# Performance work log

Measured on AMD Instinct MI355X. Metric: run time of the kernel, lower is better.

The kernel has to match this reference:

```python
import jax, jax.numpy as jnp
import numpy as np
import math

B, L, HID, H = 16, 1024, 1024, 16
E = HID // H
HALF = L // 2 + 1                      # 513 rfft bins
GLOBAL_RATIO = 0.6
LEFT = int(HALF * (1.0 - GLOBAL_RATIO))  # 205 (i=0, filter_mixer='G')
RIGHT = HALF                            # 513
FACTOR = 1
TOP_K = int(FACTOR * math.log(L))       # 6
LN_EPS = 1e-12


def setup_inputs() -> dict:
    key = jax.random.key(0)
    ks = jax.random.split(key, 12)
    s = 0.02
    return {
        "input_tensor": jax.random.normal(ks[0], (B, L, HID), jnp.float32),
        "attention_mask": jnp.zeros((B, 1, 1, L), jnp.float32),
        "Wq": jax.random.normal(ks[1], (HID, HID), jnp.float32) * s,
        "bq": jnp.zeros((HID,), jnp.float32),
        "Wk": jax.random.normal(ks[2], (HID, HID), jnp.float32) * s,
        "bk": jnp.zeros((HID,), jnp.float32),
        "Wv": jax.random.normal(ks[3], (HID, HID), jnp.float32) * s,
        "bv": jnp.zeros((HID,), jnp.float32),
        "Wd": jax.random.normal(ks[4], (HID, HID), jnp.float32) * s,
        "bd": jnp.zeros((HID,), jnp.float32),
        "gamma": jnp.ones((HID,), jnp.float32),
        "beta": jnp.zeros((HID,), jnp.float32),
    }


def _heads(x):  # [B,L,HID] -> [B,H,E,L]
    return x.reshape(B, L, H, E).transpose(0, 2, 3, 1)


def _layer_norm(x, gamma, beta):
    mu = jnp.mean(x, axis=-1, keepdims=True)
    var = jnp.var(x, axis=-1, keepdims=True)
    return (x - mu) / jnp.sqrt(var + LN_EPS) * gamma + beta


def reference(input_tensor, attention_mask, Wq, bq, Wk, bk, Wv, bv, Wd, bd, gamma, beta):
    # QKV projections -> [B,H,E,L]
    q = _heads(input_tensor @ Wq + bq)
    k = _heads(input_tensor @ Wk + bk)
    v = _heads(input_tensor @ Wv + bv)

    # FFT-based autocorrelation restricted to retained frequency band [LEFT,RIGHT)
    q_fft = jnp.fft.rfft(q, axis=-1)            # [B,H,E,HALF] complex64
    k_fft = jnp.fft.rfft(k, axis=-1)
    res = q_fft[..., LEFT:RIGHT] * jnp.conj(k_fft[..., LEFT:RIGHT])
    box = jnp.zeros((B, H, E, HALF), res.dtype).at[..., LEFT:RIGHT].set(res)
    corr = jnp.fft.irfft(box, n=L, axis=-1)     # [B,H,E,L]

    # time_delay_agg_training: topk shared delays, softmax-weighted roll aggregation
    mean_value = jnp.mean(corr, axis=(1, 2))            # [B,L]
    _, idx = jax.lax.top_k(jnp.mean(mean_value, axis=0), TOP_K)  # [TOP_K]
    weights = mean_value[:, idx]                         # [B,TOP_K]
    tmp_corr = jax.nn.softmax(weights, axis=-1)
    delays_agg = jnp.zeros_like(v)
    for i in range(TOP_K):  # TOP_K=6, fixed small loop
        pattern = jnp.roll(v, -idx[i], axis=-1)
        delays_agg = delays_agg + pattern * tmp_corr[:, i][:, None, None, None]

    # [B,H,E,L] -> [B,L,HID]
    context = delays_agg.transpose(0, 3, 1, 2).reshape(B, L, HID)
    hidden = context @ Wd + bd
    return _layer_norm(hidden + input_tensor, gamma, beta)
```

## Files before the change

### kernel.cpp

```cpp
#include <hip/hip_runtime.h>


typedef unsigned short u16;
typedef unsigned int   u32;
typedef __attribute__((ext_vector_type(8))) __bf16 bf16x8;
typedef __attribute__((ext_vector_type(4))) float  floatx4;

#define HIDn 1024

__device__ __forceinline__ u16 f2b(float f){ u32 i = __float_as_uint(f); return (u16)((i + 0x7fffu + ((i>>16)&1u)) >> 16); }

__device__ __forceinline__ void gl_lds16(const u16* g, u16* l){
  __builtin_amdgcn_global_load_lds((__attribute__((address_space(1))) const void*)g,
                                   (__attribute__((address_space(3))) void*)l, 16, 0, 0);
}

__device__ __forceinline__ void bar(){
  asm volatile("" ::: "memory");
  __builtin_amdgcn_s_barrier();
  asm volatile("" ::: "memory");
}
__device__ __forceinline__ void lgkm0(){
  asm volatile("s_waitcnt lgkmcnt(0)" ::: "memory");
  __builtin_amdgcn_sched_barrier(0);
}

__global__ void fill_kernel(float* __restrict__ out, float v, int n)
{
  const int i = blockIdx.x*blockDim.x + threadIdx.x;
  if (i < n) out[i] = v;
}

__global__ __launch_bounds__(256)
void cast_kernel(const float* __restrict__ x, u16* __restrict__ xb)
{
  const int i = blockIdx.x*256 + threadIdx.x;
  const float4* xp = (const float4*)x;
  const float4 a = xp[2*i], b = xp[2*i+1];
  uint4 o;
  o.x = (u32)f2b(a.x) | ((u32)f2b(a.y)<<16);
  o.y = (u32)f2b(a.z) | ((u32)f2b(a.w)<<16);
  o.z = (u32)f2b(b.x) | ((u32)f2b(b.y)<<16);
  o.w = (u32)f2b(b.z) | ((u32)f2b(b.w)<<16);
  ((uint4*)xb)[i] = o;
}

__global__ __launch_bounds__(1024)
void transpose_kernel(const float* __restrict__ Wq, const float* __restrict__ Wk,
                      const float* __restrict__ Wv, const float* __restrict__ Wd,
                      u16* __restrict__ WqkvT, u16* __restrict__ WdT)
{
  __shared__ float tile[32][33];
  const int mat = blockIdx.z;
  const float* W = (mat==0)?Wq:(mat==1)?Wk:(mat==2)?Wv:Wd;
  const int k = blockIdx.y*32 + threadIdx.y;
  const int n = blockIdx.x*32 + threadIdx.x;
  tile[threadIdx.y][threadIdx.x] = W[(long)k*HIDn + n];
  __syncthreads();
  const int on = blockIdx.x*32 + threadIdx.y;
  const int ok = blockIdx.y*32 + threadIdx.x;
  const u16 val = f2b(tile[threadIdx.x][threadIdx.y]);
  if (mat < 3) WqkvT[(long)(mat*HIDn + on)*HIDn + ok] = val;
  else         WdT[(long)on*HIDn + ok] = val;
}

__global__ __launch_bounds__(1024)
void gf_kernel(float* __restrict__ gf, float* __restrict__ c)
{
  const int d = threadIdx.x;
  float s = 0.f;
  for (int f = 205; f < 512; ++f){
    int p = (f*d) & 1023;
    s += cosf(6.283185307179586f * (float)p * (1.0f/1024.0f));
  }
  gf[d] = (2.f*s + ((d & 1) ? -1.f : 1.f)) * (1.0f/1048576.0f);
  #pragma unroll
  for (int b = 0; b < 16; ++b) c[b*1024 + d] = 0.f;
}

template<int EPI>
__global__ __launch_bounds__(512, 2)
void gemm_mfma(const u16* __restrict__ A, int lda, long sA,
               const u16* __restrict__ Bt, int ldb, long sB,
               void* __restrict__ C0, u16* __restrict__ o1, u16* __restrict__ o2,
               int ldc, int K,
               const float* __restrict__ b0, const float* __restrict__ b1,
               const float* __restrict__ b2, const float* __restrict__ resid,
               float* __restrict__ cbuf)
{
  __shared__ __align__(16) u16 As[2][16384];
  __shared__ __align__(16) u16 Bs[2][16384];
  __shared__ float bins[512];

  const int bx = blockIdx.x, by = blockIdx.y, bz = blockIdx.z;
  const int tid  = threadIdx.x;
  const int wave = tid >> 6, lane = tid & 63;
  const int waveM = wave >> 2, waveN = wave & 3;
  const int qd = lane >> 4, ln = lane & 15, rl = ln & 7;
  const u16* Ab = A  + (long)bz * sA;
  const u16* Bb = Bt + (long)bz * sB;
  const int aRow0 = by * 256, bRow0 = bx * 256;
  const int nt = K >> 6;

  const int s0 = wave*128 + lane;
  const int r0 = s0 >> 3, r1 = r0 + 8;
  const int kc = ((s0 & 7) ^ (r0 & 7)) * 8;
  const long aOff0 = (long)(aRow0 + r0)*lda + kc;
  const long aOff1 = (long)(aRow0 + r1)*lda + kc;
  const long bOff0 = (long)(bRow0 + r0)*ldb + kc;
  const long bOff1 = (long)(bRow0 + r1)*ldb + kc;
  const int dstW = wave*1024;

#define STAGE_A(p, h, kt) do{ \
    gl_lds16(Ab + aOff0 + (long)(h)*128*lda + (kt), &As[p][(h)*8192 + dstW]); \
    gl_lds16(Ab + aOff1 + (long)(h)*128*lda + (kt), &As[p][(h)*8192 + dstW + 512]); }while(0)
#define STAGE_B(p, h, kt) do{ \
    gl_lds16(Bb + bOff0 + (long)(h)*128*ldb + (kt), &Bs[p][(h)*8192 + dstW]); \
    gl_lds16(Bb + bOff1 + (long)(h)*128*ldb + (kt), &Bs[p][(h)*8192 + dstW + 512]); }while(0)

  if (EPI == 3) bins[tid] = 0.f;

  floatx4 acc[8][4];
  const floatx4 z4 = {0.f, 0.f, 0.f, 0.f};
  #pragma unroll
  for (int i=0;i<8;++i)
    #pragma unroll
    for (int j=0;j<4;++j) acc[i][j] = z4;

  const int aRd = (waveM*128 + ln)*64;
  const int bRd = (waveN*64  + ln)*64;
  const int csw0 = ((0 + qd) ^ rl) * 8;
  const int csw1 = ((4 + qd) ^ rl) * 8;

  STAGE_B(0,0,0); STAGE_B(0,1,0); STAGE_A(0,0,0); STAGE_A(0,1,0);
  STAGE_B(1,0,64); STAGE_B(1,1,64); STAGE_A(1,0,64);
  asm volatile("s_waitcnt vmcnt(6)" ::: "memory");
  __builtin_amdgcn_s_barrier();
  asm volatile("" ::: "memory");

  bf16x8 av[2][4], bv[2][4];
  for (int t = 0; t < nt; ++t){
    const int p = t & 1, pn = p ^ 1;
    const u16* Ap = &As[p][0];
    const u16* Bp = &Bs[p][0];
    const int k1 = (t+1) << 6, k2 = (t+2) << 6;

    #pragma unroll
    for (int mi=0;mi<4;++mi){
      av[0][mi] = *(const bf16x8*)(Ap + aRd + mi*1024 + csw0);
      av[1][mi] = *(const bf16x8*)(Ap + aRd + mi*1024 + csw1);
    }
    #pragma unroll
    for (int ni=0;ni<2;++ni){
      bv[0][ni] = *(const bf16x8*)(Bp + bRd + ni*1024 + csw0);
      bv[1][ni] = *(const bf16x8*)(Bp + bRd + ni*1024 + csw1);
    }
    if (t+1 < nt) STAGE_A(pn, 1, k1);
    bar(); lgkm0();
    __builtin_amdgcn_s_setprio(1);
    #pragma unroll
    for (int kk=0;kk<2;++kk)
      #pragma unroll
      for (int mi=0;mi<4;++mi)
        #pragma unroll
        for (int ni=0;ni<2;++ni)
          acc[mi][ni] = __builtin_amdgcn_mfma_f32_16x16x32_bf16(av[kk][mi], bv[kk][ni], acc[mi][ni], 0,0,0);
    __builtin_amdgcn_s_setprio(0);
    bar();

    #pragma unroll
    for (int ni=2;ni<4;++ni){
      bv[0][ni] = *(const bf16x8*)(Bp + bRd + ni*1024 + csw0);
      bv[1][ni] = *(const bf16x8*)(Bp + bRd + ni*1024 + csw1);
    }
    bar(); lgkm0();
    __builtin_amdgcn_s_setprio(1);
    #pragma unroll
    for (int kk=0;kk<2;++kk)
      #pragma unroll
      for (int mi=0;mi<4;++mi)
        #pragma unroll
        for (int ni=2;ni<4;++ni)
          acc[mi][ni] = __builtin_amdgcn_mfma_f32_16x16x32_bf16(av[kk][mi], bv[kk][ni], acc[mi][ni], 0,0,0);
    __builtin_amdgcn_s_setprio(0);
    bar();

    #pragma unroll
    for (int mi=0;mi<4;++mi){
      av[0][mi] = *(const bf16x8*)(Ap + aRd + 4096 + mi*1024 + csw0);
      av[1][mi] = *(const bf16x8*)(Ap + aRd + 4096 + mi*1024 + csw1);
    }
    if (t+2 < nt) STAGE_B(p, 0, k2);
    bar(); lgkm0();
    __builtin_amdgcn_s_setprio(1);
    #pragma unroll
    for (int kk=0;kk<2;++kk)
      #pragma unroll
      for (int mi=0;mi<4;++mi)
        #pragma unroll
        for (int ni=0;ni<2;++ni)
          acc[4+mi][ni] = __builtin_amdgcn_mfma_f32_16x16x32_bf16(av[kk][mi], bv[kk][ni], acc[4+mi][ni], 0,0,0);
    __builtin_amdgcn_s_setprio(0);
    bar();

    if (t+2 < nt){
      STAGE_B(p, 1, k2); STAGE_A(p, 0, k2);
      asm volatile("s_waitcnt vmcnt(6)" ::: "memory");
    } else if (t+1 < nt){
      asm volatile("s_waitcnt vmcnt(0)" ::: "memory");
    }
    bar();
    __builtin_amdgcn_s_setprio(1);
    #pragma unroll
    for (int kk=0;kk<2;++kk)
      #pragma unroll
      for (int mi=0;mi<4;++mi)
        #pragma unroll
        for (int ni=2;ni<4;++ni)
          acc[4+mi][ni] = __builtin_amdgcn_mfma_f32_16x16x32_bf16(av[kk][mi], bv[kk][ni], acc[4+mi][ni], 0,0,0);
    __builtin_amdgcn_s_setprio(0);
    bar();
  }
#undef STAGE_A
#undef STAGE_B

  if (EPI == 3){
    float dsum[11][4];
    #pragma unroll
    for (int dd=0; dd<11; ++dd)
      #pragma unroll
      for (int r=0;r<4;++r) dsum[dd][r] = 0.f;
    #pragma unroll
    for (int mi=0;mi<8;++mi)
      #pragma unroll
      for (int ni=0;ni<4;++ni){
        const int dd = mi - ni + 3;
        #pragma unroll
        for (int r=0;r<4;++r) dsum[dd][r] += acc[mi][ni][r];
      }
    const int base = 255 + 128*waveM - 64*waveN + 4*qd - ln;
    #pragma unroll
    for (int dd=0; dd<11; ++dd)
      #pragma unroll
      for (int r=0;r<4;++r)
        atomicAdd(&bins[base + 16*(dd-3) + r], dsum[dd][r]);
    __syncthreads();
    if (tid < 511){
      const int d = (aRow0 - bRow0 + tid - 255) & 1023;
      atomicAdd(cbuf + bz*1024 + d, bins[tid]);
    }
    return;
  }

  if (EPI == 0){
    const int which = bx >> 2;
    const float* bp = (which==0) ? b0 : ((which==1) ? b1 : b2);
    u16* Cb = (which==0) ? (u16*)C0 : ((which==1) ? o1 : o2);
    const int nb = bRow0 & 1023;
    #pragma unroll
    for (int mi=0;mi<8;++mi){
      const int gm = aRow0 + waveM*128 + mi*16 + qd*4;
      #pragma unroll
      for (int ni=0;ni<4;++ni){
        const int nl = nb + waveN*64 + ni*16 + ln;
        const float bias = bp[nl];
        #pragma unroll
        for (int r=0;r<4;++r) Cb[(long)(gm+r)*ldc + nl] = f2b(acc[mi][ni][r] + bias);
      }
    }
  } else {
    float* C = (float*)C0;
    #pragma unroll
    for (int mi=0;mi<8;++mi){
      const int gm = aRow0 + waveM*128 + mi*16 + qd*4;
      #pragma unroll
      for (int ni=0;ni<4;++ni){
        const int gn = bRow0 + waveN*64 + ni*16 + ln;
        const float bias = b0[gn];
        #pragma unroll
        for (int r=0;r<4;++r)
          C[(long)(gm+r)*ldc + gn] = acc[mi][ni][r] + bias + resid[(long)(gm+r)*ldc + gn];
      }
    }
  }
}

__global__ __launch_bounds__(1024)
void filter_kernel(const float* __restrict__ c, const float* __restrict__ gf,
                   float* __restrict__ mv)
{
  __shared__ float carr[1024];
  __shared__ float gsh[1024];
  const int b = blockIdx.x, l = threadIdx.x;
  carr[l] = c[b*1024 + l]; gsh[l] = gf[l];
  __syncthreads();
  float o = 0.f;
  #pragma unroll 4
  for (int m = 0; m < 1024; ++m) o += carr[m] * gsh[(l - m) & 1023];
  mv[b*1024 + l] = o;
}

__global__ __launch_bounds__(1024)
void topk_kernel(const float* __restrict__ mv, int* __restrict__ idxout,
                 float* __restrict__ wout)
{
  __shared__ float vals[1024];
  __shared__ float rv[1024];
  __shared__ int   ri[1024];
  __shared__ int   chosen[6];
  const int t = threadIdx.x;
  float s = 0.f;
  #pragma unroll
  for (int b = 0; b < 16; ++b) s += mv[b*1024 + t];
  vals[t] = s;
  __syncthreads();
  for (int r = 0; r < 6; ++r){
    rv[t] = vals[t]; ri[t] = t; __syncthreads();
    for (int off = 512; off > 0; off >>= 1){
      if (t < off){
        const float v2 = rv[t+off]; const int i2 = ri[t+off];
        if (v2 > rv[t] || (v2 == rv[t] && i2 < ri[t])){ rv[t] = v2; ri[t] = i2; }
      }
      __syncthreads();
    }
    if (t == 0){ chosen[r] = ri[0]; idxout[r] = ri[0]; }
    __syncthreads();
    if (t == chosen[r]) vals[t] = -3.0e38f;
    __syncthreads();
  }
  if (t < 16){
    float w[6]; float mx = -3.0e38f;
    #pragma unroll
    for (int i = 0; i < 6; ++i){ w[i] = mv[t*1024 + chosen[i]]; mx = fmaxf(mx, w[i]); }
    float sum = 0.f;
    #pragma unroll
    for (int i = 0; i < 6; ++i){ w[i] = expf(w[i] - mx); sum += w[i]; }
    #pragma unroll
    for (int i = 0; i < 6; ++i) wout[t*6 + i] = w[i] / sum;
  }
}

__global__ __launch_bounds__(256)
void context_kernel(const u16* __restrict__ Vb, const int* __restrict__ idx,
                    const float* __restrict__ w, u16* __restrict__ CT)
{
  const int row = blockIdx.x*2 + (threadIdx.x >> 7);
  const int b = row >> 10, l = row & 1023;
  const int t = threadIdx.x & 127;
  float wl[6]; int id[6];
  #pragma unroll
  for (int i = 0; i < 6; ++i){ id[i] = idx[i]; wl[i] = w[b*6 + i]; }
  float acc[8] = {0,0,0,0,0,0,0,0};
  #pragma unroll
  for (int i = 0; i < 6; ++i){
    const long src = (long)b*1024 + ((l + id[i]) & 1023);
    const uint4 pk = *(const uint4*)(Vb + src*1024 + t*8);
    const float ww = wl[i];
    union{float f; u32 u;} cv;
    cv.u = pk.x<<16;          acc[0] += ww*cv.f;
    cv.u = pk.x & 0xffff0000u; acc[1] += ww*cv.f;
    cv.u = pk.y<<16;          acc[2] += ww*cv.f;
    cv.u = pk.y & 0xffff0000u; acc[3] += ww*cv.f;
    cv.u = pk.z<<16;          acc[4] += ww*cv.f;
    cv.u = pk.z & 0xffff0000u; acc[5] += ww*cv.f;
    cv.u = pk.w<<16;          acc[6] += ww*cv.f;
    cv.u = pk.w & 0xffff0000u; acc[7] += ww*cv.f;
  }
  uint4 o;
  o.x = (u32)f2b(acc[0]) | ((u32)f2b(acc[1])<<16);
  o.y = (u32)f2b(acc[2]) | ((u32)f2b(acc[3])<<16);
  o.z = (u32)f2b(acc[4]) | ((u32)f2b(acc[5])<<16);
  o.w = (u32)f2b(acc[6]) | ((u32)f2b(acc[7])<<16);
  *(uint4*)(CT + (long)row*1024 + t*8) = o;
}

__global__ __launch_bounds__(256)
void ln_kernel(float* __restrict__ io, const float* __restrict__ gamma,
               const float* __restrict__ beta)
{
  __shared__ float s1[256];
  __shared__ float s2[256];
  const int row = blockIdx.x, t = threadIdx.x;
  float4 v = ((const float4*)(io + (long)row*1024))[t];
  s1[t] = v.x+v.y+v.z+v.w;
  s2[t] = v.x*v.x+v.y*v.y+v.z*v.z+v.w*v.w;
  __syncthreads();
  for (int off = 128; off > 0; off >>= 1){
    if (t < off){ s1[t] += s1[t+off]; s2[t] += s2[t+off]; }
    __syncthreads();
  }
  const float mu  = s1[0] * (1.f/1024.f);
  const float var = fmaxf(s2[0] * (1.f/1024.f) - mu*mu, 0.f);
  const float rstd = rsqrtf(var + 1e-12f);
  const float4 g  = ((const float4*)gamma)[t];
  const float4 be = ((const float4*)beta)[t];
  float4 o;
  o.x = (v.x-mu)*rstd*g.x + be.x;
  o.y = (v.y-mu)*rstd*g.y + be.y;
  o.z = (v.z-mu)*rstd*g.z + be.z;
  o.w = (v.w-mu)*rstd*g.w + be.w;
  ((float4*)(io + (long)row*1024))[t] = o;
}

extern "C" void kernel_launch(void* const* d_in, const int* in_sizes, int n_in,
                              void* d_out, int out_size, void* d_ws, size_t ws_size,
                              hipStream_t stream)
{
  (void)in_sizes; (void)n_in;
  const float* x     = (const float*)d_in[0];
  const float* Wq    = (const float*)d_in[2];
  const float* bq    = (const float*)d_in[3];
  const float* Wk    = (const float*)d_in[4];
  const float* bk    = (const float*)d_in[5];
  const float* Wv    = (const float*)d_in[6];
  const float* bv    = (const float*)d_in[7];
  const float* Wd    = (const float*)d_in[8];
  const float* bd    = (const float*)d_in[9];
  const float* gamma = (const float*)d_in[10];
  const float* beta  = (const float*)d_in[11];
  float* outp = (float*)d_out;

  const size_t NEED = 142741952UL;
  if (ws_size < NEED){
    const int n = out_size/2;
    fill_kernel<<<(n+255)/256, 256, 0, stream>>>(outp, (float)ws_size, n);
    return;
  }
  char* ws = (char*)d_ws;
  u16*  xb    = (u16*)(ws);
  u16*  Qb    = (u16*)(ws + 33554432L);
  u16*  Kb    = (u16*)(ws + 67108864L);
  u16*  Vb    = (u16*)(ws + 100663296L);
  u16*  WqkvT = (u16*)(ws + 134217728L);
  u16*  WdT   = (u16*)(ws + 140509184L);
  float* cbuf = (float*)(ws + 142606336L);
  float* mv   = (float*)(ws + 142671872L);
  float* gf   = (float*)(ws + 142737408L);
  int*   idxb = (int*)  (ws + 142741504L);
  float* wsm  = (float*)(ws + 142741568L);
  u16*  CT    = Qb;

  cast_kernel<<<8192, 256, 0, stream>>>(x, xb);
  transpose_kernel<<<dim3(32,32,4), dim3(32,32), 0, stream>>>(Wq, Wk, Wv, Wd, WqkvT, WdT);
  gf_kernel<<<1, 1024, 0, stream>>>(gf, cbuf);

  gemm_mfma<0><<<dim3(12,64,1), 512, 0, stream>>>(
      xb, 1024, 0L, WqkvT, 1024, 0L, Qb, Kb, Vb, 1024, 1024,
      bq, bk, bv, nullptr, nullptr);

  gemm_mfma<3><<<dim3(4,4,16), 512, 0, stream>>>(
      Qb, 1024, 1048576L, Kb, 1024, 1048576L, nullptr, nullptr, nullptr, 0, 1024,
      nullptr, nullptr, nullptr, nullptr, cbuf);

  filter_kernel<<<16, 1024, 0, stream>>>(cbuf, gf, mv);
  topk_kernel<<<1, 1024, 0, stream>>>(mv, idxb, wsm);
  context_kernel<<<8192, 256, 0, stream>>>(Vb, idxb, wsm, CT);

  gemm_mfma<2><<<dim3(4,64,1), 512, 0, stream>>>(
      CT, 1024, 0L, WdT, 1024, 0L, outp, nullptr, nullptr, 1024, 1024,
      bd, nullptr, nullptr, x, nullptr);

  ln_kernel<<<16384, 256, 0, stream>>>(outp, gamma, beta);
}
```

Measured before the change: 497.7 us.

## Restructure GEMM main loop to prefetch LDS fragments across MFMA phases with fewer barriers

Rewrites the inner K-loop of the bf16 MFMA GEMM so each phase computes a full 4x4 tile over one k-half, loading the next k-half's fragments while the current MFMAs issue. The first fragments of the next tile are loaded ahead of the final phase. This cuts the number of workgroup barriers per iteration and overlaps LDS reads with matrix math, replacing the per-phase lgkmcnt waits with sched_barrier-ordered issue. In exchange it keeps more fragment registers live, which may raise register pressure, and it relies on subtle buffer-reuse ordering between STAGE writes and the reads of the previous tile.

```diff
diff --git a/kernel.cpp b/kernel.cpp
--- a/kernel.cpp
+++ b/kernel.cpp
@@ -19,10 +19,6 @@
   asm volatile("" ::: "memory");
   __builtin_amdgcn_s_barrier();
   asm volatile("" ::: "memory");
-}
-__device__ __forceinline__ void lgkm0(){
-  asm volatile("s_waitcnt lgkmcnt(0)" ::: "memory");
-  __builtin_amdgcn_sched_barrier(0);
 }
 
 __global__ void fill_kernel(float* __restrict__ out, float v, int n)
@@ -138,69 +134,68 @@
   __builtin_amdgcn_s_barrier();
   asm volatile("" ::: "memory");
 
-  bf16x8 av[2][4], bv[2][4];
+  bf16x8 avA[4], avB[4], bvA[4], bvB[4];
+  {
+    const u16* Ap = &As[0][0]; const u16* Bp = &Bs[0][0];
+    avA[0] = *(const bf16x8*)(Ap + aRd + 0*1024 + csw0);
+    #pragma unroll
+    for (int ni=0;ni<4;++ni) bvA[ni] = *(const bf16x8*)(Bp + bRd + ni*1024 + csw0);
+    #pragma unroll
+    for (int mi=1;mi<4;++mi) avA[mi] = *(const bf16x8*)(Ap + aRd + mi*1024 + csw0);
+  }
+  __builtin_amdgcn_sched_barrier(0);
+
   for (int t = 0; t < nt; ++t){
-    const int p = t & 1, pn = p ^ 1;
+    const int p = t & 1;
     const u16* Ap = &As[p][0];
     const u16* Bp = &Bs[p][0];
     const int k1 = (t+1) << 6, k2 = (t+2) << 6;
 
+    __builtin_amdgcn_s_setprio(1);
     #pragma unroll
     for (int mi=0;mi<4;++mi){
-      av[0][mi] = *(const bf16x8*)(Ap + aRd + mi*1024 + csw0);
-      av[1][mi] = *(const bf16x8*)(Ap + aRd + mi*1024 + csw1);
-    }
-    #pragma unroll
-    for (int ni=0;ni<2;++ni){
-      bv[0][ni] = *(const bf16x8*)(Bp + bRd + ni*1024 + csw0);
-      bv[1][ni] = *(const bf16x8*)(Bp + bRd + ni*1024 + csw1);
-    }
-    if (t+1 < nt) STAGE_A(pn, 1, k1);
-    bar(); lgkm0();
+      #pragma unroll
+      for (int ni=0;ni<4;++ni)
+        acc[mi][ni] = __builtin_amdgcn_mfma_f32_16x16x32_bf16(avA[mi], bvA[ni], acc[mi][ni], 0,0,0);
+      __builtin_amdgcn_sched_barrier(0);
+    }
+    __builtin_amdgcn_s_setprio(0);
+
+    avB[0] = *(const bf16x8*)(Ap + aRd + 0*1024 + csw1);
+    #pragma unroll
+    for (int ni=0;ni<4;++ni) bvB[ni] = *(const bf16x8*)(Bp + bRd + ni*1024 + csw1);
+    #pragma unroll
+    for (int mi=1;mi<4;++mi) avB[mi] = *(const bf16x8*)(Ap + aRd + mi*1024 + csw1);
+    if (t+1 < nt) STAGE_A(p^1, 1, k1);
+    __builtin_amdgcn_sched_barrier(0);
     __builtin_amdgcn_s_setprio(1);
     #pragma unroll
-    for (int kk=0;kk<2;++kk)
-      #pragma unroll
-      for (int mi=0;mi<4;++mi)
-        #pragma unroll
-        for (int ni=0;ni<2;++ni)
-          acc[mi][ni] = __builtin_amdgcn_mfma_f32_16x16x32_bf16(av[kk][mi], bv[kk][ni], acc[mi][ni], 0,0,0);
+    for (int mi=0;mi<4;++mi){
+      #pragma unroll
+      for (int ni=0;ni<4;++ni)
+        acc[mi][ni] = __builtin_amdgcn_mfma_f32_16x16x32_bf16(avB[mi], bvB[ni], acc[mi][ni], 0,0,0);
+      __builtin_amdgcn_sched_barrier(0);
+    }
     __builtin_amdgcn_s_setprio(0);
     bar();
 
     #pragma unroll
-    for (int ni=2;ni<4;++ni){
-      bv[0][ni] = *(const bf16x8*)(Bp + bRd + ni*1024 + csw0);
-      bv[1][ni] = *(const bf16x8*)(Bp + bRd + ni*1024 + csw1);
-    }
-    bar(); lgkm0();
+    for (int mi=0;mi<4;++mi) avA[mi] = *(const bf16x8*)(Ap + aRd + 4096 + mi*1024 + csw0);
+    #pragma unroll
+    for (int mi=0;mi<4;++mi) avB[mi] = *(const bf16x8*)(Ap + aRd + 4096 + mi*1024 + csw1);
+    if (t+2 < nt) STAGE_B(p, 0, k2);
+    __builtin_amdgcn_sched_barrier(0);
     __builtin_amdgcn_s_setprio(1);
     #pragma unroll
-    for (int kk=0;kk<2;++kk)
-      #pragma unroll
-      for (int mi=0;mi<4;++mi)
-        #pragma unroll
-        for (int ni=2;ni<4;++ni)
-          acc[mi][ni] = __builtin_amdgcn_mfma_f32_16x16x32_bf16(av[kk][mi], bv[kk][ni], acc[mi][ni], 0,0,0);
+    for (int mi=0;mi<4;++mi){
+      #pragma unroll
+      for (int ni=0;ni<4;++ni)
+        acc[4+mi][ni] = __builtin_amdgcn_mfma_f32_16x16x32_bf16(avA[mi], bvA[ni], acc[4+mi][ni], 0,0,0);
+      __builtin_amdgcn_sched_barrier(0);
+    }
     __builtin_amdgcn_s_setprio(0);
-    bar();
-
-    #pragma unroll
-    for (int mi=0;mi<4;++mi){
-      av[0][mi] = *(const bf16x8*)(Ap + aRd + 4096 + mi*1024 + csw0);
-      av[1][mi] = *(const bf16x8*)(Ap + aRd + 4096 + mi*1024 + csw1);
-    }
-    if (t+2 < nt) STAGE_B(p, 0, k2);
-    bar(); lgkm0();
-    __builtin_amdgcn_s_setprio(1);
-    #pragma unroll
-    for (int kk=0;kk<2;++kk)
-      #pragma unroll
-      for (int mi=0;mi<4;++mi)
-        #pragma unroll
-        for (int ni=0;ni<2;++ni)
-          acc[4+mi][ni] = __builtin_amdgcn_mfma_f32_16x16x32_bf16(av[kk][mi], bv[kk][ni], acc[4+mi][ni], 0,0,0);
-    __builtin_amdgcn_s_setprio(0);
+    asm volatile("s_waitcnt lgkmcnt(0)" ::: "memory");
+    __builtin_amdgcn_sched_barrier(0);
     bar();
 
     if (t+2 < nt){
@@ -209,17 +204,26 @@
     } else if (t+1 < nt){
       asm volatile("s_waitcnt vmcnt(0)" ::: "memory");
     }
-    bar();
+    if (t+1 < nt){
+      bar();
+      const u16* An = &As[p^1][0];
+      const u16* Bn = &Bs[p^1][0];
+      avA[0] = *(const bf16x8*)(An + aRd + 0*1024 + csw0);
+      #pragma unroll
+      for (int ni=0;ni<4;++ni) bvA[ni] = *(const bf16x8*)(Bn + bRd + ni*1024 + csw0);
+      #pragma unroll
+      for (int mi=1;mi<4;++mi) avA[mi] = *(const bf16x8*)(An + aRd + mi*1024 + csw0);
+      __builtin_amdgcn_sched_barrier(0);
+    }
     __builtin_amdgcn_s_setprio(1);
     #pragma unroll
-    for (int kk=0;kk<2;++kk)
-      #pragma unroll
-      for (int mi=0;mi<4;++mi)
-        #pragma unroll
-        for (int ni=2;ni<4;++ni)
-          acc[4+mi][ni] = __builtin_amdgcn_mfma_f32_16x16x32_bf16(av[kk][mi], bv[kk][ni], acc[4+mi][ni], 0,0,0);
+    for (int mi=0;mi<4;++mi){
+      #pragma unroll
+      for (int ni=0;ni<4;++ni)
+        acc[4+mi][ni] = __builtin_amdgcn_mfma_f32_16x16x32_bf16(avB[mi], bvB[ni], acc[4+mi][ni], 0,0,0);
+      __builtin_amdgcn_sched_barrier(0);
+    }
     __builtin_amdgcn_s_setprio(0);
-    bar();
   }
 #undef STAGE_A
 #undef STAGE_B
```

Result: no change. 499.0 us (+0.3%).
